# Kernel optimization log

Measured on AMD Instinct MI355X. Metric: run time of the kernel, lower is better.

The kernel has to match this reference:

```python
import jax, jax.numpy as jnp
import numpy as np

D, H, L, FF = 512, 8, 6, 2048
EPS = 1e-5


def _ln(x, g, b):
    m = x.mean(-1, keepdims=True)
    v = ((x - m) ** 2).mean(-1, keepdims=True)
    return (x - m) * jax.lax.rsqrt(v + EPS) * g + b


def _mha(qi, ki, vi, w, b):
    # w: [4, D, D] (q, k, v, out), b: [4, D]; weights stored [in, out]
    B, Sq, _ = qi.shape
    Sk = ki.shape[1]
    dk = D // H
    q = (qi @ w[0] + b[0]).reshape(B, Sq, H, dk)
    k = (ki @ w[1] + b[1]).reshape(B, Sk, H, dk)
    v = (vi @ w[2] + b[2]).reshape(B, Sk, H, dk)
    scores = jnp.einsum('bqhd,bkhd->bhqk', q, k) / np.float32(np.sqrt(dk))
    attn = jax.nn.softmax(scores, axis=-1)
    o = jnp.einsum('bhqk,bkhd->bqhd', attn, v).reshape(B, Sq, D)
    return o @ w[3] + b[3]


def setup_inputs() -> dict:
    key = jax.random.key(0)
    ks = jax.random.split(key, 12)
    bs, c, h, w = 4, D, 32, 32
    nq = 100
    s = np.float32(0.02)
    f32 = jnp.float32
    return {
        'src': jax.random.normal(ks[0], (bs, c, h, w), f32),
        'query_embed': jax.random.normal(ks[1], (nq, D), f32),
        'pos_embed': jax.random.normal(ks[2], (bs, c, h, w), f32),
        # encoder params (stacked over L layers)
        'enc_attn_w': jax.random.normal(ks[3], (L, 4, D, D), f32) * s,
        'enc_attn_b': jnp.zeros((L, 4, D), f32),
        'enc_w1': jax.random.normal(ks[4], (L, D, FF), f32) * s,
        'enc_b1': jnp.zeros((L, FF), f32),
        'enc_w2': jax.random.normal(ks[5], (L, FF, D), f32) * s,
        'enc_b2': jnp.zeros((L, D), f32),
        'enc_ln_w': jnp.ones((L, 2, D), f32),
        'enc_ln_b': jnp.zeros((L, 2, D), f32),
        # decoder params
        'dec_sa_w': jax.random.normal(ks[6], (L, 4, D, D), f32) * s,
        'dec_sa_b': jnp.zeros((L, 4, D), f32),
        'dec_ca_w': jax.random.normal(ks[7], (L, 4, D, D), f32) * s,
        'dec_ca_b': jnp.zeros((L, 4, D), f32),
        'dec_w1': jax.random.normal(ks[8], (L, D, FF), f32) * s,
        'dec_b1': jnp.zeros((L, FF), f32),
        'dec_w2': jax.random.normal(ks[9], (L, FF, D), f32) * s,
        'dec_b2': jnp.zeros((L, D), f32),
        'dec_ln_w': jnp.ones((L, 3, D), f32),
        'dec_ln_b': jnp.zeros((L, 3, D), f32),
    }


def reference(src, query_embed, pos_embed,
              enc_attn_w, enc_attn_b, enc_w1, enc_b1, enc_w2, enc_b2,
              enc_ln_w, enc_ln_b,
              dec_sa_w, dec_sa_b, dec_ca_w, dec_ca_b,
              dec_w1, dec_b1, dec_w2, dec_b2, dec_ln_w, dec_ln_b):
    bs, c, h, w = src.shape
    x = src.reshape(bs, c, h * w).transpose(0, 2, 1)        # [B, HW, D]
    pos = pos_embed.reshape(bs, c, h * w).transpose(0, 2, 1)  # [B, HW, D]
    qe = jnp.broadcast_to(query_embed[None], (bs,) + query_embed.shape)  # [B, NQ, D]

    def enc_step(mem, p):
        aw, ab, w1, b1, w2, b2, lnw, lnb = p
        t = mem + pos  # original re-adds pos_embed every encoder layer
        t = _ln(t + _mha(t, t, t, aw, ab), lnw[0], lnb[0])
        f = jax.nn.relu(t @ w1 + b1) @ w2 + b2
        t = _ln(t + f, lnw[1], lnb[1])
        return t, None

    memory, _ = jax.lax.scan(
        enc_step, x,
        (enc_attn_w, enc_attn_b, enc_w1, enc_b1, enc_w2, enc_b2, enc_ln_w, enc_ln_b))

    mem_in = memory + pos

    def dec_step(out, p):
        saw, sab, caw, cab, w1, b1, w2, b2, lnw, lnb = p
        t = out + qe  # original re-adds query_embed every decoder layer
        t = _ln(t + _mha(t, t, t, saw, sab), lnw[0], lnb[0])
        t = _ln(t + _mha(t, mem_in, mem_in, caw, cab), lnw[1], lnb[1])
        f = jax.nn.relu(t @ w1 + b1) @ w2 + b2
        t = _ln(t + f, lnw[2], lnb[2])
        return t, None

    tgt = jnp.zeros_like(qe)
    output, _ = jax.lax.scan(
        dec_step, tgt,
        (dec_sa_w, dec_sa_b, dec_ca_w, dec_ca_b, dec_w1, dec_b1, dec_w2, dec_b2,
         dec_ln_w, dec_ln_b))
    return output, memory
```

## Files before the change

### kernel.cpp

```cpp
#include <hip/hip_runtime.h>
#include <math.h>


typedef unsigned short bfu;
typedef unsigned int u32;
typedef __bf16 bf8v __attribute__((ext_vector_type(8)));
typedef float f32x4 __attribute__((ext_vector_type(4)));

__device__ inline bfu f2bf(float f) {
  union { float f; u32 u; } v; v.f = f;
  u32 u = v.u;
  u32 r = (u + 0x7fffu + ((u >> 16) & 1u)) >> 16;
  return (bfu)r;
}
__device__ inline float bflo(u32 u) { return __uint_as_float(u << 16); }

typedef const __attribute__((address_space(1))) u32 gas_t;
typedef __attribute__((address_space(3))) u32 las_t;
__device__ __forceinline__ void gl16(const void* g, void* l) {
  __builtin_amdgcn_global_load_lds((gas_t*)g, (las_t*)l, 16, 0, 0);
}

__global__ __launch_bounds__(256) void k_transpose2(const float* __restrict__ s0,
                                                    const float* __restrict__ s1,
                                                    float* __restrict__ d0,
                                                    float* __restrict__ d1) {
  __shared__ float tile[32][33];
  int zz = blockIdx.z;
  const float* in = (zz < 4) ? s0 : s1;
  float* out = (zz < 4) ? d0 : d1;
  int b = zz & 3;
  int c0 = blockIdx.x * 32, s0i = blockIdx.y * 32;
  int tx = threadIdx.x, ty = threadIdx.y;
  for (int i = ty; i < 32; i += 8)
    tile[i][tx] = in[((size_t)(b * 512 + c0 + i)) * 1024 + s0i + tx];
  __syncthreads();
  for (int i = ty; i < 32; i += 8)
    out[((size_t)(b * 1024 + s0i + i)) * 512 + c0 + tx] = tile[tx][i];
}

__global__ __launch_bounds__(256) void k_wt(const float* __restrict__ src,
                                            bfu* __restrict__ dst,
                                            int K, int N) {
  __shared__ bfu tile[32][33];
  int g = blockIdx.z;
  const float* s = src + (size_t)g * (size_t)K * N;
  bfu* d = dst + (size_t)g * (size_t)K * N;
  int n0 = blockIdx.x * 32, k0 = blockIdx.y * 32;
  int tx = threadIdx.x, ty = threadIdx.y;
  for (int i = ty; i < 32; i += 8)
    tile[i][tx] = f2bf(s[(size_t)(k0 + i) * N + n0 + tx]);
  __syncthreads();
  for (int i = ty; i < 32; i += 8)
    d[(size_t)(n0 + i) * K + k0 + tx] = tile[tx][i];
}

__global__ void k_add_dual(const float* __restrict__ a, const float* __restrict__ b,
                           float* __restrict__ of, bfu* __restrict__ ob, int n4) {
  int i = blockIdx.x * blockDim.x + threadIdx.x;
  if (i >= n4) return;
  float4 x = ((const float4*)a)[i];
  float4 y = ((const float4*)b)[i];
  float4 r = make_float4(x.x + y.x, x.y + y.y, x.z + y.z, x.w + y.w);
  ((float4*)of)[i] = r;
  ((ushort4*)ob)[i] = make_ushort4(f2bf(r.x), f2bf(r.y), f2bf(r.z), f2bf(r.w));
}

__global__ void k_qe0(const float* __restrict__ qe, float* __restrict__ of,
                      bfu* __restrict__ ob) {
  int i = blockIdx.x * blockDim.x + threadIdx.x;
  if (i >= 51200) return;
  int row = i >> 7;
  int q = row % 100;
  int c4 = i & 127;
  float4 y = ((const float4*)qe)[q * 128 + c4];
  ((float4*)of)[i] = y;
  ((ushort4*)ob)[i] = make_ushort4(f2bf(y.x), f2bf(y.y), f2bf(y.z), f2bf(y.w));
}

__global__ __launch_bounds__(256) void k_ln_red(const float* __restrict__ A,
                                                const float* __restrict__ P,
                                                int nsplit, size_t pz,
                                                const float* __restrict__ bias,
                                                const float* __restrict__ g,
                                                const float* __restrict__ be,
                                                float* __restrict__ of,
                                                bfu* __restrict__ ob,
                                                const float* __restrict__ add2,
                                                int qe_mode,
                                                float* __restrict__ of2,
                                                bfu* __restrict__ ob2,
                                                int rows) {
  int row = blockIdx.x * 4 + (threadIdx.x >> 6);
  int lane = threadIdx.x & 63;
  if (row >= rows) return;
  const float* pa = A + (size_t)row * 512;
  float v[8];
  float s = 0.f, s2 = 0.f;
#pragma unroll
  for (int j = 0; j < 8; ++j) {
    int c = lane + j * 64;
    float x = pa[c] + bias[c];
    for (int z = 0; z < nsplit; ++z) x += P[z * pz + (size_t)row * 512 + c];
    v[j] = x; s += x; s2 += x * x;
  }
#pragma unroll
  for (int off = 32; off > 0; off >>= 1) {
    s += __shfl_xor(s, off);
    s2 += __shfl_xor(s2, off);
  }
  float mean = s * (1.f / 512.f);
  float var = s2 * (1.f / 512.f) - mean * mean;
  float r = rsqrtf(var + 1e-5f);
  int arow = qe_mode ? (row % 100) : row;
#pragma unroll
  for (int j = 0; j < 8; ++j) {
    int c = lane + j * 64;
    float o = (v[j] - mean) * r * g[c] + be[c];
    if (of) of[(size_t)row * 512 + c] = o;
    if (ob) ob[(size_t)row * 512 + c] = f2bf(o);
    if (add2) {
      float o2 = o + add2[(size_t)arow * 512 + c];
      if (of2) of2[(size_t)row * 512 + c] = o2;
      if (ob2) ob2[(size_t)row * 512 + c] = f2bf(o2);
    }
  }
}

__global__ __launch_bounds__(256) void k_gemm_bf(const bfu* __restrict__ A,
                                                 const bfu* __restrict__ Wt,
                                                 const float* __restrict__ bias,
                                                 bfu* __restrict__ C,
                                                 int M, int N, int K, int relu,
                                                 size_t wtz, size_t cz, int bz) {
  __shared__ bfu As[2][128][64];
  __shared__ bfu Bs[2][128][64];
  int z = blockIdx.z;
  Wt += (size_t)z * wtz; C += (size_t)z * cz; bias += z * bz;
  int bm = blockIdx.y * 128, bn = blockIdx.x * 128;
  int t = threadIdx.x;
  int wave = t >> 6, lane = t & 63;
  int wm = wave >> 1, wn = wave & 1;
  int l15 = lane & 15, l4 = lane >> 4;
  f32x4 acc[4][4];
  f32x4 zz = {0.f, 0.f, 0.f, 0.f};
#pragma unroll
  for (int mi = 0; mi < 4; ++mi)
#pragma unroll
    for (int ni = 0; ni < 4; ++ni) acc[mi][ni] = zz;

  auto stage = [&](int buf, int k0) {
#pragma unroll
    for (int i = 0; i < 4; ++i) {
      int c = t + i * 256;
      int row = c >> 3, kg = c & 7;
      int sc = kg ^ (row & 7);
      if (bm + row < M)
        gl16(A + (size_t)(bm + row) * K + k0 + sc * 8, &As[buf][row][kg * 8]);
      gl16(Wt + (size_t)(bn + row) * K + k0 + sc * 8, &Bs[buf][row][kg * 8]);
    }
  };
  stage(0, 0);
  int cur = 0;
  for (int k0 = 0; k0 < K; k0 += 64) {
    __syncthreads();
    if (k0 + 64 < K) stage(cur ^ 1, k0 + 64);
#pragma unroll
    for (int kc = 0; kc < 2; ++kc) {
      bf8v av[4], bv[4];
#pragma unroll
      for (int mi = 0; mi < 4; ++mi) {
        int row = wm * 64 + mi * 16 + l15;
        av[mi] = *(const bf8v*)&As[cur][row][((kc * 4 + l4) ^ (row & 7)) * 8];
      }
#pragma unroll
      for (int ni = 0; ni < 4; ++ni) {
        int row = wn * 64 + ni * 16 + l15;
        bv[ni] = *(const bf8v*)&Bs[cur][row][((kc * 4 + l4) ^ (row & 7)) * 8];
      }
#pragma unroll
      for (int mi = 0; mi < 4; ++mi)
#pragma unroll
        for (int ni = 0; ni < 4; ++ni)
          acc[mi][ni] = __builtin_amdgcn_mfma_f32_16x16x32_bf16(av[mi], bv[ni],
                                                                acc[mi][ni], 0, 0, 0);
    }
    cur ^= 1;
  }

#pragma unroll
  for (int mi = 0; mi < 4; ++mi) {
    int row0 = bm + wm * 64 + mi * 16 + l4 * 4;
#pragma unroll
    for (int ni = 0; ni < 4; ++ni) {
      int col = bn + wn * 64 + ni * 16 + l15;
      float bb = bias[col];
#pragma unroll
      for (int r = 0; r < 4; ++r) {
        int row = row0 + r;
        if (row < M) {
          float v = acc[mi][ni][r] + bb;
          if (relu) v = fmaxf(v, 0.f);
          C[(size_t)row * N + col] = f2bf(v);
        }
      }
    }
  }
}

__global__ __launch_bounds__(256) void k_gemm_sk(const bfu* __restrict__ A,
                                                 const bfu* __restrict__ Wt,
                                                 float* __restrict__ Pf,
                                                 int M, int N, int K, int ksplit) {
  __shared__ bfu As[2][128][64];
  __shared__ bfu Bs[2][128][64];
  int z = blockIdx.z;
  int Kc = K / ksplit;
  int kbeg = z * Kc;
  Pf += (size_t)z * M * N;
  int bm = blockIdx.y * 128, bn = blockIdx.x * 128;
  int t = threadIdx.x;
  int wave = t >> 6, lane = t & 63;
  int wm = wave >> 1, wn = wave & 1;
  int l15 = lane & 15, l4 = lane >> 4;
  f32x4 acc[4][4];
  f32x4 zz = {0.f, 0.f, 0.f, 0.f};
#pragma unroll
  for (int mi = 0; mi < 4; ++mi)
#pragma unroll
    for (int ni = 0; ni < 4; ++ni) acc[mi][ni] = zz;

  auto stage = [&](int buf, int k0) {
#pragma unroll
    for (int i = 0; i < 4; ++i) {
      int c = t + i * 256;
      int row = c >> 3, kg = c & 7;
      int sc = kg ^ (row & 7);
      if (bm + row < M)
        gl16(A + (size_t)(bm + row) * K + k0 + sc * 8, &As[buf][row][kg * 8]);
      gl16(Wt + (size_t)(bn + row) * K + k0 + sc * 8, &Bs[buf][row][kg * 8]);
    }
  };
  stage(0, kbeg);
  int cur = 0;
  for (int k0 = kbeg; k0 < kbeg + Kc; k0 += 64) {
    __syncthreads();
    if (k0 + 64 < kbeg + Kc) stage(cur ^ 1, k0 + 64);
#pragma unroll
    for (int kc = 0; kc < 2; ++kc) {
      bf8v av[4], bv[4];
#pragma unroll
      for (int mi = 0; mi < 4; ++mi) {
        int row = wm * 64 + mi * 16 + l15;
        av[mi] = *(const bf8v*)&As[cur][row][((kc * 4 + l4) ^ (row & 7)) * 8];
      }
#pragma unroll
      for (int ni = 0; ni < 4; ++ni) {
        int row = wn * 64 + ni * 16 + l15;
        bv[ni] = *(const bf8v*)&Bs[cur][row][((kc * 4 + l4) ^ (row & 7)) * 8];
      }
#pragma unroll
      for (int mi = 0; mi < 4; ++mi)
#pragma unroll
        for (int ni = 0; ni < 4; ++ni)
          acc[mi][ni] = __builtin_amdgcn_mfma_f32_16x16x32_bf16(av[mi], bv[ni],
                                                                acc[mi][ni], 0, 0, 0);
    }
    cur ^= 1;
  }

#pragma unroll
  for (int mi = 0; mi < 4; ++mi) {
    int row0 = bm + wm * 64 + mi * 16 + l4 * 4;
#pragma unroll
    for (int ni = 0; ni < 4; ++ni) {
      int col = bn + wn * 64 + ni * 16 + l15;
#pragma unroll
      for (int r = 0; r < 4; ++r) {
        int row = row0 + r;
        if (row < M) Pf[(size_t)row * N + col] = acc[mi][ni][r];
      }
    }
  }
}

__global__ __launch_bounds__(256) void k_attn_mfma(const bfu* __restrict__ Q, int qs,
                                                   const bfu* __restrict__ Km,
                                                   const bfu* __restrict__ Vm, int kvs,
                                                   bfu* __restrict__ O,
                                                   int Sq, int Sk) {
  __shared__ bfu Ks[128][72];
  __shared__ bfu Vt[64][136];
  __shared__ bfu Sm[4][16][136];
  const float scale = 0.125f;
  int b = blockIdx.z, h = blockIdx.y;
  int q0 = blockIdx.x * 64;
  int t = threadIdx.x;
  int wave = t >> 6, lane = t & 63;
  int l15 = lane & 15, l4 = lane >> 4;
  int hoff = h * 64;

  uint4 uq0 = {0u, 0u, 0u, 0u}, uq1 = {0u, 0u, 0u, 0u};
  {
    int qrow = q0 + wave * 16 + l15;
    if (qrow < Sq) {
      const bfu* qp = Q + (size_t)(b * Sq + qrow) * qs + hoff + l4 * 8;
      uq0 = *(const uint4*)qp;
      uq1 = *(const uint4*)(qp + 32);
    }
  }
  bf8v qf0 = *(bf8v*)&uq0, qf1 = *(bf8v*)&uq1;

  float m_[4] = {-1e30f, -1e30f, -1e30f, -1e30f};
  float l_[4] = {0.f, 0.f, 0.f, 0.f};
  f32x4 oacc[4];
  f32x4 zz = {0.f, 0.f, 0.f, 0.f};
#pragma unroll
  for (int n = 0; n < 4; ++n) oacc[n] = zz;

  uint4 ruk[4], ruv[4];
  const uint4 uz = {0u, 0u, 0u, 0u};
  auto load_kv = [&](int k0) {
#pragma unroll
    for (int i = 0; i < 4; ++i) {
      int e = t + i * 256;
      int rk = e >> 3, cg = e & 7;
      ruk[i] = uz;
      if (k0 + rk < Sk)
        ruk[i] = *(const uint4*)(Km + (size_t)(b * Sk + k0 + rk) * kvs + hoff + cg * 8);
      int kv = e & 127, dg = e >> 7;
      ruv[i] = uz;
      if (k0 + kv < Sk)
        ruv[i] = *(const uint4*)(Vm + (size_t)(b * Sk + k0 + kv) * kvs + hoff + dg * 8);
    }
  };
  load_kv(0);

  for (int k0 = 0; k0 < Sk; k0 += 128) {
#pragma unroll
    for (int i = 0; i < 4; ++i) {
      int e = t + i * 256;
      int rk = e >> 3, cg = e & 7;
      *(uint4*)&Ks[rk][cg * 8] = ruk[i];
      int kv = e & 127, dg = e >> 7;
      bfu vv[8];
      *(uint4*)vv = ruv[i];
#pragma unroll
      for (int j = 0; j < 8; ++j) Vt[dg * 8 + j][kv] = vv[j];
    }
    __syncthreads();
    if (k0 + 128 < Sk) load_kv(k0 + 128);

    f32x4 s4[8];
    __builtin_amdgcn_s_setprio(1);
#pragma unroll
    for (int tt = 0; tt < 8; ++tt) {
      bf8v kf0 = *(const bf8v*)&Ks[tt * 16 + l15][l4 * 8];
      bf8v kf1 = *(const bf8v*)&Ks[tt * 16 + l15][32 + l4 * 8];
      f32x4 a = zz;
      a = __builtin_amdgcn_mfma_f32_16x16x32_bf16(qf0, kf0, a, 0, 0, 0);
      a = __builtin_amdgcn_mfma_f32_16x16x32_bf16(qf1, kf1, a, 0, 0, 0);
      s4[tt] = a;
    }
    __builtin_amdgcn_s_setprio(0);

    float f_[4];
#pragma unroll
    for (int r = 0; r < 4; ++r) {
      float sv[8];
      float mx = -1e30f;
#pragma unroll
      for (int tt = 0; tt < 8; ++tt) {
        float s = s4[tt][r] * scale;
        s = (k0 + tt * 16 + l15 < Sk) ? s : -1e30f;
        sv[tt] = s;
        mx = fmaxf(mx, s);
      }
#pragma unroll
      for (int off = 1; off < 16; off <<= 1) mx = fmaxf(mx, __shfl_xor(mx, off));
      float nm = fmaxf(m_[r], mx);
      float f = __expf(m_[r] - nm);
      float ps = 0.f;
#pragma unroll
      for (int tt = 0; tt < 8; ++tt) {
        float p = __expf(sv[tt] - nm);
        ps += p;
        Sm[wave][l4 * 4 + r][tt * 16 + l15] = f2bf(p);
      }
#pragma unroll
      for (int off = 1; off < 16; off <<= 1) ps += __shfl_xor(ps, off);
      l_[r] = l_[r] * f + ps;
      m_[r] = nm;
      f_[r] = f;
    }
#pragma unroll
    for (int n = 0; n < 4; ++n)
#pragma unroll
      for (int r = 0; r < 4; ++r) oacc[n][r] *= f_[r];

    __builtin_amdgcn_s_setprio(1);
#pragma unroll
    for (int h2 = 0; h2 < 2; ++h2) {
      bf8v p0 = *(const bf8v*)&Sm[wave][l15][h2 * 64 + l4 * 8];
      bf8v p1 = *(const bf8v*)&Sm[wave][l15][h2 * 64 + 32 + l4 * 8];
#pragma unroll
      for (int n = 0; n < 4; ++n) {
        bf8v v0 = *(const bf8v*)&Vt[n * 16 + l15][h2 * 64 + l4 * 8];
        bf8v v1 = *(const bf8v*)&Vt[n * 16 + l15][h2 * 64 + 32 + l4 * 8];
        oacc[n] = __builtin_amdgcn_mfma_f32_16x16x32_bf16(p0, v0, oacc[n], 0, 0, 0);
        oacc[n] = __builtin_amdgcn_mfma_f32_16x16x32_bf16(p1, v1, oacc[n], 0, 0, 0);
      }
    }
    __builtin_amdgcn_s_setprio(0);
    __syncthreads();
  }

#pragma unroll
  for (int r = 0; r < 4; ++r) {
    int row = q0 + wave * 16 + l4 * 4 + r;
    if (row < Sq) {
      float inv = 1.f / l_[r];
#pragma unroll
      for (int n = 0; n < 4; ++n)
        O[(size_t)(b * Sq + row) * 512 + hoff + n * 16 + l15] = f2bf(oacc[n][r] * inv);
    }
  }
}


extern "C" void kernel_launch(void* const* d_in, const int* in_sizes, int n_in,
                              void* d_out, int out_size, void* d_ws, size_t ws_size,
                              hipStream_t stream) {
  const float* src         = (const float*)d_in[0];
  const float* query_embed = (const float*)d_in[1];
  const float* pos_embed   = (const float*)d_in[2];
  const float* enc_attn_w  = (const float*)d_in[3];
  const float* enc_attn_b  = (const float*)d_in[4];
  const float* enc_w1      = (const float*)d_in[5];
  const float* enc_b1      = (const float*)d_in[6];
  const float* enc_w2      = (const float*)d_in[7];
  const float* enc_b2      = (const float*)d_in[8];
  const float* enc_ln_w    = (const float*)d_in[9];
  const float* enc_ln_b    = (const float*)d_in[10];
  const float* dec_sa_w    = (const float*)d_in[11];
  const float* dec_sa_b    = (const float*)d_in[12];
  const float* dec_ca_w    = (const float*)d_in[13];
  const float* dec_ca_b    = (const float*)d_in[14];
  const float* dec_w1      = (const float*)d_in[15];
  const float* dec_b1      = (const float*)d_in[16];
  const float* dec_w2      = (const float*)d_in[17];
  const float* dec_b2      = (const float*)d_in[18];
  const float* dec_ln_w    = (const float*)d_in[19];
  const float* dec_ln_b    = (const float*)d_in[20];
  float* out = (float*)d_out;

  const size_t ENC = 4UL * 1024 * 512;
  const size_t DEC = 4UL * 100 * 512;
  const size_t MAT = 512UL * 512;

  float* p = (float*)d_ws;
  float* x    = p; p += ENC;
  float* pos  = p; p += ENC;
  float* t1   = p; p += ENC;
  float* t2   = p; p += ENC;
  float* t3   = p; p += DEC;
  float* Pf   = p; p += 4 * ENC;

  bfu* bp = (bfu*)p;
  bfu* t1b    = bp; bp += ENC;
  bfu* t2b    = bp; bp += ENC;
  bfu* t3b    = bp; bp += DEC;
  bfu* qkvb   = bp; bp += 4096UL * 1536;
  bfu* aob    = bp; bp += ENC;
  bfu* hbb    = bp; bp += 4096UL * 2048;
  bfu* meminb = bp; bp += ENC;
  bfu* ckvb   = bp; bp += 6UL * 4096 * 1024;
  bfu* enc_att_t = bp; bp += 24 * MAT;
  bfu* enc_w1t   = bp; bp += 6UL * 512 * 2048;
  bfu* enc_w2t   = bp; bp += 6UL * 2048 * 512;
  bfu* dsa_t     = bp; bp += 24 * MAT;
  bfu* dca_t     = bp; bp += 24 * MAT;
  bfu* dw1t      = bp; bp += 6UL * 512 * 2048;
  bfu* dw2t      = bp; bp += 6UL * 2048 * 512;

  dim3 tb(32, 8);
  k_transpose2<<<dim3(16, 32, 8), tb, 0, stream>>>(src, pos_embed, x, pos);

  k_wt<<<dim3(16, 16, 24), tb, 0, stream>>>(enc_attn_w, enc_att_t, 512, 512);
  k_wt<<<dim3(64, 16, 6),  tb, 0, stream>>>(enc_w1,     enc_w1t,   512, 2048);
  k_wt<<<dim3(16, 64, 6),  tb, 0, stream>>>(enc_w2,     enc_w2t,   2048, 512);
  k_wt<<<dim3(16, 16, 24), tb, 0, stream>>>(dec_sa_w,   dsa_t,     512, 512);
  k_wt<<<dim3(16, 16, 24), tb, 0, stream>>>(dec_ca_w,   dca_t,     512, 512);
  k_wt<<<dim3(64, 16, 6),  tb, 0, stream>>>(dec_w1,     dw1t,      512, 2048);
  k_wt<<<dim3(16, 64, 6),  tb, 0, stream>>>(dec_w2,     dw2t,      2048, 512);

  k_add_dual<<<2048, 256, 0, stream>>>(x, pos, t1, t1b, (int)(ENC / 4));
  for (int l = 0; l < 6; ++l) {
    const bfu* awt = enc_att_t + (size_t)l * 4 * MAT;
    const float* ab = enc_attn_b + (size_t)l * 2048;
    k_gemm_bf<<<dim3(12, 32), 256, 0, stream>>>(t1b, awt, ab,
                                                qkvb, 4096, 1536, 512, 0, 0, 0, 0);
    k_attn_mfma<<<dim3(16, 8, 4), 256, 0, stream>>>(qkvb, 1536, qkvb + 512, qkvb + 1024, 1536,
                                                    aob, 1024, 1024);
    k_gemm_sk<<<dim3(4, 32, 2), 256, 0, stream>>>(aob, awt + 3 * MAT, Pf,
                                                  4096, 512, 512, 2);
    k_ln_red<<<1024, 256, 0, stream>>>(t1, Pf, 2, ENC, ab + 1536,
                                       enc_ln_w + (size_t)(l * 2 + 0) * 512,
                                       enc_ln_b + (size_t)(l * 2 + 0) * 512,
                                       t2, t2b, (const float*)nullptr, 0,
                                       (float*)nullptr, (bfu*)nullptr, 4096);
    k_gemm_bf<<<dim3(16, 32), 256, 0, stream>>>(t2b, enc_w1t + (size_t)l * 512 * 2048,
                                                enc_b1 + (size_t)l * 2048, hbb,
                                                4096, 2048, 512, 1, 0, 0, 0);
    k_gemm_sk<<<dim3(4, 32, 4), 256, 0, stream>>>(hbb, enc_w2t + (size_t)l * 2048 * 512, Pf,
                                                  4096, 512, 2048, 4);
    if (l < 5) {
      k_ln_red<<<1024, 256, 0, stream>>>(t2, Pf, 4, ENC, enc_b2 + (size_t)l * 512,
                                         enc_ln_w + (size_t)(l * 2 + 1) * 512,
                                         enc_ln_b + (size_t)(l * 2 + 1) * 512,
                                         (float*)nullptr, (bfu*)nullptr,
                                         pos, 0, t1, t1b, 4096);
    } else {
      k_ln_red<<<1024, 256, 0, stream>>>(t2, Pf, 4, ENC, enc_b2 + (size_t)l * 512,
                                         enc_ln_w + (size_t)(l * 2 + 1) * 512,
                                         enc_ln_b + (size_t)(l * 2 + 1) * 512,
                                         out + DEC, (bfu*)nullptr,
                                         pos, 0, (float*)nullptr, meminb, 4096);
    }
  }

  k_gemm_bf<<<dim3(8, 32, 6), 256, 0, stream>>>(meminb, dca_t + MAT, dec_ca_b + 512,
                                                ckvb, 4096, 1024, 512, 0,
                                                4 * MAT, 4096UL * 1024, 2048);

  k_qe0<<<200, 256, 0, stream>>>(query_embed, t1, t1b);
  for (int l = 0; l < 6; ++l) {
    const bfu* swt = dsa_t + (size_t)l * 4 * MAT;
    const bfu* cwt = dca_t + (size_t)l * 4 * MAT;
    const float* sb = dec_sa_b + (size_t)l * 2048;
    const float* cb = dec_ca_b + (size_t)l * 2048;
    k_gemm_bf<<<dim3(12, 4), 256, 0, stream>>>(t1b, swt, sb,
                                               qkvb, 400, 1536, 512, 0, 0, 0, 0);
    k_attn_mfma<<<dim3(2, 8, 4), 256, 0, stream>>>(qkvb, 1536, qkvb + 512, qkvb + 1024, 1536,
                                                   aob, 100, 100);
    k_gemm_sk<<<dim3(4, 4, 2), 256, 0, stream>>>(aob, swt + 3 * MAT, Pf,
                                                 400, 512, 512, 2);
    k_ln_red<<<100, 256, 0, stream>>>(t1, Pf, 2, 400UL * 512, sb + 1536,
                                      dec_ln_w + (size_t)(l * 3 + 0) * 512,
                                      dec_ln_b + (size_t)(l * 3 + 0) * 512,
                                      t2, t2b, (const float*)nullptr, 0,
                                      (float*)nullptr, (bfu*)nullptr, 400);
    k_gemm_bf<<<dim3(4, 4), 256, 0, stream>>>(t2b, cwt, cb,
                                              qkvb, 400, 512, 512, 0, 0, 0, 0);
    k_attn_mfma<<<dim3(2, 8, 4), 256, 0, stream>>>(qkvb, 512,
                                                   ckvb + (size_t)l * 4096 * 1024,
                                                   ckvb + (size_t)l * 4096 * 1024 + 512, 1024,
                                                   aob, 100, 1024);
    k_gemm_sk<<<dim3(4, 4, 2), 256, 0, stream>>>(aob, cwt + 3 * MAT, Pf,
                                                 400, 512, 512, 2);
    k_ln_red<<<100, 256, 0, stream>>>(t2, Pf, 2, 400UL * 512, cb + 1536,
                                      dec_ln_w + (size_t)(l * 3 + 1) * 512,
                                      dec_ln_b + (size_t)(l * 3 + 1) * 512,
                                      t3, t3b, (const float*)nullptr, 0,
                                      (float*)nullptr, (bfu*)nullptr, 400);
    k_gemm_bf<<<dim3(16, 4), 256, 0, stream>>>(t3b, dw1t + (size_t)l * 512 * 2048,
                                               dec_b1 + (size_t)l * 2048, hbb,
                                               400, 2048, 512, 1, 0, 0, 0);
    k_gemm_sk<<<dim3(4, 4, 4), 256, 0, stream>>>(hbb, dw2t + (size_t)l * 2048 * 512, Pf,
                                                 400, 512, 2048, 4);
    if (l < 5) {
      k_ln_red<<<100, 256, 0, stream>>>(t3, Pf, 4, 400UL * 512, dec_b2 + (size_t)l * 512,
                                        dec_ln_w + (size_t)(l * 3 + 2) * 512,
                                        dec_ln_b + (size_t)(l * 3 + 2) * 512,
                                        (float*)nullptr, (bfu*)nullptr,
                                        query_embed, 1, t1, t1b, 400);
    } else {
      k_ln_red<<<100, 256, 0, stream>>>(t3, Pf, 4, 400UL * 512, dec_b2 + (size_t)l * 512,
                                        dec_ln_w + (size_t)(l * 3 + 2) * 512,
                                        dec_ln_b + (size_t)(l * 3 + 2) * 512,
                                        out, (bfu*)nullptr,
                                        (const float*)nullptr, 0,
                                        (float*)nullptr, (bfu*)nullptr, 400);
    }
  }
}
```

Measured before the change: 1.952 ms.

## Halve GEMM K-tile, merge weight-transpose launches, skip masking on full attention tiles

Both bf16 MFMA GEMM kernels now stage 32-wide K tiles instead of 64. The LDS swizzle is adapted to the narrower rows, LDS use is halved and more blocks can fit per CU, at the cost of twice as many barrier iterations. The seven weight-transpose launches are merged into three launches that select among source tensors by blockIdx.z, cutting launch overhead. The attention softmax skips the per-element Sk bound check when a key tile is fully in range.

```diff
diff --git a/kernel.cpp b/kernel.cpp
--- a/kernel.cpp
+++ b/kernel.cpp
@@ -39,12 +39,16 @@
     out[((size_t)(b * 1024 + s0i + i)) * 512 + c0 + tx] = tile[tx][i];
 }
 
-__global__ __launch_bounds__(256) void k_wt(const float* __restrict__ src,
-                                            bfu* __restrict__ dst,
-                                            int K, int N) {
+__global__ __launch_bounds__(256) void k_wt3(const float* __restrict__ s0,
+                                             const float* __restrict__ s1,
+                                             const float* __restrict__ s2,
+                                             bfu* __restrict__ dst,
+                                             int K, int N, int per) {
   __shared__ bfu tile[32][33];
   int g = blockIdx.z;
-  const float* s = src + (size_t)g * (size_t)K * N;
+  const float* sb = (g < per) ? s0 : (g < 2 * per) ? s1 : s2;
+  int gl = (g < per) ? g : (g < 2 * per) ? (g - per) : (g - 2 * per);
+  const float* s = sb + (size_t)gl * (size_t)K * N;
   bfu* d = dst + (size_t)g * (size_t)K * N;
   int n0 = blockIdx.x * 32, k0 = blockIdx.y * 32;
   int tx = threadIdx.x, ty = threadIdx.y;
@@ -133,8 +137,8 @@
                                                  bfu* __restrict__ C,
                                                  int M, int N, int K, int relu,
                                                  size_t wtz, size_t cz, int bz) {
-  __shared__ bfu As[2][128][64];
-  __shared__ bfu Bs[2][128][64];
+  __shared__ bfu As[2][128][32];
+  __shared__ bfu Bs[2][128][32];
   int z = blockIdx.z;
   Wt += (size_t)z * wtz; C += (size_t)z * cz; bias += z * bz;
   int bm = blockIdx.y * 128, bn = blockIdx.x * 128;
@@ -151,10 +155,10 @@
 
   auto stage = [&](int buf, int k0) {
 #pragma unroll
-    for (int i = 0; i < 4; ++i) {
+    for (int i = 0; i < 2; ++i) {
       int c = t + i * 256;
-      int row = c >> 3, kg = c & 7;
-      int sc = kg ^ (row & 7);
+      int row = c >> 2, kg = c & 3;
+      int sc = kg ^ ((row >> 2) & 3);
       if (bm + row < M)
         gl16(A + (size_t)(bm + row) * K + k0 + sc * 8, &As[buf][row][kg * 8]);
       gl16(Wt + (size_t)(bn + row) * K + k0 + sc * 8, &Bs[buf][row][kg * 8]);
@@ -162,29 +166,26 @@
   };
   stage(0, 0);
   int cur = 0;
-  for (int k0 = 0; k0 < K; k0 += 64) {
+  for (int k0 = 0; k0 < K; k0 += 32) {
     __syncthreads();
-    if (k0 + 64 < K) stage(cur ^ 1, k0 + 64);
-#pragma unroll
-    for (int kc = 0; kc < 2; ++kc) {
-      bf8v av[4], bv[4];
-#pragma unroll
-      for (int mi = 0; mi < 4; ++mi) {
-        int row = wm * 64 + mi * 16 + l15;
-        av[mi] = *(const bf8v*)&As[cur][row][((kc * 4 + l4) ^ (row & 7)) * 8];
-      }
-#pragma unroll
-      for (int ni = 0; ni < 4; ++ni) {
-        int row = wn * 64 + ni * 16 + l15;
-        bv[ni] = *(const bf8v*)&Bs[cur][row][((kc * 4 + l4) ^ (row & 7)) * 8];
-      }
-#pragma unroll
-      for (int mi = 0; mi < 4; ++mi)
-#pragma unroll
-        for (int ni = 0; ni < 4; ++ni)
-          acc[mi][ni] = __builtin_amdgcn_mfma_f32_16x16x32_bf16(av[mi], bv[ni],
-                                                                acc[mi][ni], 0, 0, 0);
-    }
+    if (k0 + 32 < K) stage(cur ^ 1, k0 + 32);
+    bf8v av[4], bv[4];
+#pragma unroll
+    for (int mi = 0; mi < 4; ++mi) {
+      int row = wm * 64 + mi * 16 + l15;
+      av[mi] = *(const bf8v*)&As[cur][row][(l4 ^ ((row >> 2) & 3)) * 8];
+    }
+#pragma unroll
+    for (int ni = 0; ni < 4; ++ni) {
+      int row = wn * 64 + ni * 16 + l15;
+      bv[ni] = *(const bf8v*)&Bs[cur][row][(l4 ^ ((row >> 2) & 3)) * 8];
+    }
+#pragma unroll
+    for (int mi = 0; mi < 4; ++mi)
+#pragma unroll
+      for (int ni = 0; ni < 4; ++ni)
+        acc[mi][ni] = __builtin_amdgcn_mfma_f32_16x16x32_bf16(av[mi], bv[ni],
+                                                              acc[mi][ni], 0, 0, 0);
     cur ^= 1;
   }
 
@@ -212,8 +213,8 @@
                                                  const bfu* __restrict__ Wt,
                                                  float* __restrict__ Pf,
                                                  int M, int N, int K, int ksplit) {
-  __shared__ bfu As[2][128][64];
-  __shared__ bfu Bs[2][128][64];
+  __shared__ bfu As[2][128][32];
+  __shared__ bfu Bs[2][128][32];
   int z = blockIdx.z;
   int Kc = K / ksplit;
   int kbeg = z * Kc;
@@ -232,10 +233,10 @@
 
   auto stage = [&](int buf, int k0) {
 #pragma unroll
-    for (int i = 0; i < 4; ++i) {
+    for (int i = 0; i < 2; ++i) {
       int c = t + i * 256;
-      int row = c >> 3, kg = c & 7;
-      int sc = kg ^ (row & 7);
+      int row = c >> 2, kg = c & 3;
+      int sc = kg ^ ((row >> 2) & 3);
       if (bm + row < M)
         gl16(A + (size_t)(bm + row) * K + k0 + sc * 8, &As[buf][row][kg * 8]);
       gl16(Wt + (size_t)(bn + row) * K + k0 + sc * 8, &Bs[buf][row][kg * 8]);
@@ -243,29 +244,26 @@
   };
   stage(0, kbeg);
   int cur = 0;
-  for (int k0 = kbeg; k0 < kbeg + Kc; k0 += 64) {
+  for (int k0 = kbeg; k0 < kbeg + Kc; k0 += 32) {
     __syncthreads();
-    if (k0 + 64 < kbeg + Kc) stage(cur ^ 1, k0 + 64);
-#pragma unroll
-    for (int kc = 0; kc < 2; ++kc) {
-      bf8v av[4], bv[4];
-#pragma unroll
-      for (int mi = 0; mi < 4; ++mi) {
-        int row = wm * 64 + mi * 16 + l15;
-        av[mi] = *(const bf8v*)&As[cur][row][((kc * 4 + l4) ^ (row & 7)) * 8];
-      }
-#pragma unroll
-      for (int ni = 0; ni < 4; ++ni) {
-        int row = wn * 64 + ni * 16 + l15;
-        bv[ni] = *(const bf8v*)&Bs[cur][row][((kc * 4 + l4) ^ (row & 7)) * 8];
-      }
-#pragma unroll
-      for (int mi = 0; mi < 4; ++mi)
-#pragma unroll
-        for (int ni = 0; ni < 4; ++ni)
-          acc[mi][ni] = __builtin_amdgcn_mfma_f32_16x16x32_bf16(av[mi], bv[ni],
-                                                                acc[mi][ni], 0, 0, 0);
-    }
+    if (k0 + 32 < kbeg + Kc) stage(cur ^ 1, k0 + 32);
+    bf8v av[4], bv[4];
+#pragma unroll
+    for (int mi = 0; mi < 4; ++mi) {
+      int row = wm * 64 + mi * 16 + l15;
+      av[mi] = *(const bf8v*)&As[cur][row][(l4 ^ ((row >> 2) & 3)) * 8];
+    }
+#pragma unroll
+    for (int ni = 0; ni < 4; ++ni) {
+      int row = wn * 64 + ni * 16 + l15;
+      bv[ni] = *(const bf8v*)&Bs[cur][row][(l4 ^ ((row >> 2) & 3)) * 8];
+    }
+#pragma unroll
+    for (int mi = 0; mi < 4; ++mi)
+#pragma unroll
+      for (int ni = 0; ni < 4; ++ni)
+        acc[mi][ni] = __builtin_amdgcn_mfma_f32_16x16x32_bf16(av[mi], bv[ni],
+                                                              acc[mi][ni], 0, 0, 0);
     cur ^= 1;
   }
 
@@ -364,17 +362,27 @@
     }
     __builtin_amdgcn_s_setprio(0);
 
+    bool full = (k0 + 128 <= Sk);
     float f_[4];
 #pragma unroll
     for (int r = 0; r < 4; ++r) {
       float sv[8];
       float mx = -1e30f;
-#pragma unroll
-      for (int tt = 0; tt < 8; ++tt) {
-        float s = s4[tt][r] * scale;
-        s = (k0 + tt * 16 + l15 < Sk) ? s : -1e30f;
-        sv[tt] = s;
-        mx = fmaxf(mx, s);
+      if (full) {
+#pragma unroll
+        for (int tt = 0; tt < 8; ++tt) {
+          float s = s4[tt][r] * scale;
+          sv[tt] = s;
+          mx = fmaxf(mx, s);
+        }
+      } else {
+#pragma unroll
+        for (int tt = 0; tt < 8; ++tt) {
+          float s = s4[tt][r] * scale;
+          s = (k0 + tt * 16 + l15 < Sk) ? s : -1e30f;
+          sv[tt] = s;
+          mx = fmaxf(mx, s);
+        }
       }
 #pragma unroll
       for (int off = 1; off < 16; off <<= 1) mx = fmaxf(mx, __shfl_xor(mx, off));
@@ -475,24 +483,26 @@
   bfu* hbb    = bp; bp += 4096UL * 2048;
   bfu* meminb = bp; bp += ENC;
   bfu* ckvb   = bp; bp += 6UL * 4096 * 1024;
-  bfu* enc_att_t = bp; bp += 24 * MAT;
-  bfu* enc_w1t   = bp; bp += 6UL * 512 * 2048;
-  bfu* enc_w2t   = bp; bp += 6UL * 2048 * 512;
-  bfu* dsa_t     = bp; bp += 24 * MAT;
-  bfu* dca_t     = bp; bp += 24 * MAT;
-  bfu* dw1t      = bp; bp += 6UL * 512 * 2048;
-  bfu* dw2t      = bp; bp += 6UL * 2048 * 512;
+  bfu* att_all_t = bp; bp += 72 * MAT;
+  bfu* w1_all_t  = bp; bp += 12UL * 512 * 2048;
+  bfu* w2_all_t  = bp; bp += 12UL * 2048 * 512;
+  bfu* enc_att_t = att_all_t;
+  bfu* dsa_t     = att_all_t + 24 * MAT;
+  bfu* dca_t     = att_all_t + 48 * MAT;
+  bfu* enc_w1t   = w1_all_t;
+  bfu* dw1t      = w1_all_t + 6UL * 512 * 2048;
+  bfu* enc_w2t   = w2_all_t;
+  bfu* dw2t      = w2_all_t + 6UL * 2048 * 512;
 
   dim3 tb(32, 8);
   k_transpose2<<<dim3(16, 32, 8), tb, 0, stream>>>(src, pos_embed, x, pos);
 
-  k_wt<<<dim3(16, 16, 24), tb, 0, stream>>>(enc_attn_w, enc_att_t, 512, 512);
-  k_wt<<<dim3(64, 16, 6),  tb, 0, stream>>>(enc_w1,     enc_w1t,   512, 2048);
-  k_wt<<<dim3(16, 64, 6),  tb, 0, stream>>>(enc_w2,     enc_w2t,   2048, 512);
-  k_wt<<<dim3(16, 16, 24), tb, 0, stream>>>(dec_sa_w,   dsa_t,     512, 512);
-  k_wt<<<dim3(16, 16, 24), tb, 0, stream>>>(dec_ca_w,   dca_t,     512, 512);
-  k_wt<<<dim3(64, 16, 6),  tb, 0, stream>>>(dec_w1,     dw1t,      512, 2048);
-  k_wt<<<dim3(16, 64, 6),  tb, 0, stream>>>(dec_w2,     dw2t,      2048, 512);
+  k_wt3<<<dim3(16, 16, 72), tb, 0, stream>>>(enc_attn_w, dec_sa_w, dec_ca_w,
+                                             att_all_t, 512, 512, 24);
+  k_wt3<<<dim3(64, 16, 12), tb, 0, stream>>>(enc_w1, dec_w1, dec_w1,
+                                             w1_all_t, 512, 2048, 6);
+  k_wt3<<<dim3(16, 64, 12), tb, 0, stream>>>(enc_w2, dec_w2, dec_w2,
+                                             w2_all_t, 2048, 512, 6);
 
   k_add_dual<<<2048, 256, 0, stream>>>(x, pos, t1, t1b, (int)(ENC / 4));
   for (int l = 0; l < 6; ++l) {
```

Measured after the change: 2.067 ms. +5.9%, slower.
